# Performance work log

Measured on AMD Instinct MI355X. Metric: run time of the kernel, lower is better.

The kernel has to match this reference:

```python
import jax, jax.numpy as jnp
import numpy as np

DROPOUT_P = 0.0  # undefined global `dropout_p` in source; pinned to 0 (identity) for determinism


def setup_inputs() -> dict:
    key = jax.random.key(0)
    k1, k2, k3 = jax.random.split(key, 3)
    B, Lq, Lk, D = 16, 4096, 4096, 64
    return {
        "query": jax.random.normal(k1, (B, Lq, D), dtype=jnp.float32),
        "key": jax.random.normal(k2, (B, Lk, D), dtype=jnp.float32),
        "value": jax.random.normal(k3, (B, Lk, D), dtype=jnp.float32),
        "scale_factor": jnp.ones((1,), dtype=jnp.float32),
    }


def reference(query, key, value, scale_factor):
    # scores: [B, Lq, Lk] -- the large HBM-materialized intermediate
    scores = jnp.einsum("bqd,bkd->bqk", query, key) / scale_factor
    probs = jax.nn.softmax(scores, axis=-1)
    # dropout with p = DROPOUT_P = 0.0 is the identity
    out = jnp.einsum("bqk,bkd->bqd", probs, value)
    return out
```

## Files before the change

kernel.cpp:

```cpp
#include <hip/hip_runtime.h>
#include <hip/hip_fp16.h>

typedef _Float16 half4_t __attribute__((ext_vector_type(4)));
typedef _Float16 half8_t __attribute__((ext_vector_type(8)));
typedef float   float4_t __attribute__((ext_vector_type(4)));

namespace {
constexpr int kB      = 16;
constexpr int kL      = 4096;
constexpr int kD      = 64;
constexpr int kQTile  = 128;
constexpr int kWQ     = 32;
constexpr int kBK     = 64;
constexpr int kStride = 72;
}

__global__ __launch_bounds__(256, 3)
void fa_fwd(const float* __restrict__ Q, const float* __restrict__ K,
            const float* __restrict__ V, const float* __restrict__ scale_ptr,
            float* __restrict__ Out)
{
    __shared__ __align__(16) _Float16 Ksh[kBK * kStride];
    __shared__ __align__(16) _Float16 Vsh[kD * kStride];

    const int tid  = threadIdx.x;
    const int wave = tid >> 6;
    const int lane = tid & 63;
    const int c    = lane & 15;
    const int qd   = lane >> 4;

    const int b  = blockIdx.y;
    const int q0 = blockIdx.x * kQTile + wave * kWQ;

    const float qscale = 1.4426950408889634f / scale_ptr[0];

    const float* Qb = Q + (size_t)b * kL * kD;
    const float* Kb = K + (size_t)b * kL * kD;
    const float* Vb = V + (size_t)b * kL * kD;

    half8_t qfrag[2][2];
#pragma unroll
    for (int qt = 0; qt < 2; ++qt) {
        const float* qrow = Qb + (size_t)(q0 + qt * 16 + c) * kD;
#pragma unroll
        for (int dk = 0; dk < 2; ++dk) {
            const float* p = qrow + dk * 32 + qd * 8;
            half8_t h;
#pragma unroll
            for (int j = 0; j < 8; ++j) h[j] = (_Float16)(p[j] * qscale);
            qfrag[qt][dk] = h;
        }
    }

    float4_t O[2][4];
#pragma unroll
    for (int qt = 0; qt < 2; ++qt)
#pragma unroll
        for (int dt = 0; dt < 4; ++dt) O[qt][dt] = (float4_t)0.0f;

    float m_run[2] = {-__builtin_inff(), -__builtin_inff()};
    float l_run[2] = {0.0f, 0.0f};

    for (int kb = 0; kb < kL; kb += kBK) {
        __syncthreads();

#pragma unroll
        for (int i = 0; i < 4; ++i) {
            const int task = tid + 256 * i;
            const int c4   = task & 15;
            const int row  = task >> 4;
            const float4 f = *(const float4*)(Kb + (size_t)(kb + row) * kD + c4 * 4);
            half4_t h;
            h[0] = (_Float16)f.x; h[1] = (_Float16)f.y;
            h[2] = (_Float16)f.z; h[3] = (_Float16)f.w;
            *(half4_t*)(&Ksh[row * kStride + c4 * 4]) = h;
        }
#pragma unroll
        for (int i = 0; i < 4; ++i) {
            const int task = tid + 256 * i;
            const int row  = task & 63;
            const int c4   = task >> 6;
            const float4 f = *(const float4*)(Vb + (size_t)(kb + row) * kD + c4 * 4);
            Vsh[(c4 * 4 + 0) * kStride + row] = (_Float16)f.x;
            Vsh[(c4 * 4 + 1) * kStride + row] = (_Float16)f.y;
            Vsh[(c4 * 4 + 2) * kStride + row] = (_Float16)f.z;
            Vsh[(c4 * 4 + 3) * kStride + row] = (_Float16)f.w;
        }
        __syncthreads();

        half8_t kf[4][2];
#pragma unroll
        for (int kt = 0; kt < 4; ++kt)
#pragma unroll
            for (int dk = 0; dk < 2; ++dk)
                kf[kt][dk] = *(const half8_t*)(&Ksh[(kt * 16 + c) * kStride + dk * 32 + qd * 8]);

        float4_t S[4][2];
#pragma unroll
        for (int kt = 0; kt < 4; ++kt)
#pragma unroll
            for (int qt = 0; qt < 2; ++qt) {
                float4_t acc = (float4_t)0.0f;
                acc = __builtin_amdgcn_mfma_f32_16x16x32_f16(kf[kt][0], qfrag[qt][0], acc, 0, 0, 0);
                acc = __builtin_amdgcn_mfma_f32_16x16x32_f16(kf[kt][1], qfrag[qt][1], acc, 0, 0, 0);
                S[kt][qt] = acc;
            }

        float alpha[2];
#pragma unroll
        for (int qt = 0; qt < 2; ++qt) {
            float tm = S[0][qt][0];
#pragma unroll
            for (int kt = 0; kt < 4; ++kt)
#pragma unroll
                for (int r = 0; r < 4; ++r) tm = fmaxf(tm, S[kt][qt][r]);
            tm = fmaxf(tm, __shfl_xor(tm, 16));
            tm = fmaxf(tm, __shfl_xor(tm, 32));
            const float mn = fmaxf(m_run[qt], tm);
            alpha[qt] = __builtin_amdgcn_exp2f(m_run[qt] - mn);
            m_run[qt] = mn;
            float rs = 0.0f;
#pragma unroll
            for (int kt = 0; kt < 4; ++kt)
#pragma unroll
                for (int r = 0; r < 4; ++r) {
                    const float pv = __builtin_amdgcn_exp2f(S[kt][qt][r] - mn);
                    S[kt][qt][r] = pv;
                    rs += pv;
                }
            rs += __shfl_xor(rs, 16);
            rs += __shfl_xor(rs, 32);
            l_run[qt] = l_run[qt] * alpha[qt] + rs;
        }

#pragma unroll
        for (int qt = 0; qt < 2; ++qt)
#pragma unroll
            for (int r = 0; r < 4; ++r) {
                const float a = __shfl(alpha[qt], qd * 4 + r);
#pragma unroll
                for (int dt = 0; dt < 4; ++dt) O[qt][dt][r] *= a;
            }

        half4_t pf[4][2];
#pragma unroll
        for (int kt = 0; kt < 4; ++kt)
#pragma unroll
            for (int qt = 0; qt < 2; ++qt) {
                half4_t h;
                h[0] = (_Float16)S[kt][qt][0]; h[1] = (_Float16)S[kt][qt][1];
                h[2] = (_Float16)S[kt][qt][2]; h[3] = (_Float16)S[kt][qt][3];
                pf[kt][qt] = h;
            }

#pragma unroll
        for (int kt = 0; kt < 4; ++kt)
#pragma unroll
            for (int dt = 0; dt < 4; ++dt) {
                const half4_t vf = *(const half4_t*)(&Vsh[(dt * 16 + c) * kStride + kt * 16 + qd * 4]);
#pragma unroll
                for (int qt = 0; qt < 2; ++qt)
                    O[qt][dt] = __builtin_amdgcn_mfma_f32_16x16x16f16(pf[kt][qt], vf, O[qt][dt], 0, 0, 0);
            }
    }

#pragma unroll
    for (int qt = 0; qt < 2; ++qt)
#pragma unroll
        for (int r = 0; r < 4; ++r) {
            const float lr  = __shfl(l_run[qt], qd * 4 + r);
            const float inv = 1.0f / lr;
            const int qrow  = q0 + qt * 16 + qd * 4 + r;
            float* op = Out + ((size_t)b * kL + qrow) * kD;
#pragma unroll
            for (int dt = 0; dt < 4; ++dt)
                op[dt * 16 + c] = O[qt][dt][r] * inv;
        }
}

extern "C" void kernel_launch(void* const* d_in, const int* in_sizes, int n_in,
                              void* d_out, int out_size, void* d_ws, size_t ws_size,
                              hipStream_t stream) {
    const float* Q = (const float*)d_in[0];
    const float* K = (const float*)d_in[1];
    const float* V = (const float*)d_in[2];
    const float* s = (const float*)d_in[3];
    float* out = (float*)d_out;
    dim3 grid(kL / kQTile, kB, 1);
    dim3 block(256, 1, 1);
    fa_fwd<<<grid, block, 0, stream>>>(Q, K, V, s, out);
}
```

Baseline: 228.8 us.

## Split query tile across eight waves and skip rescale when row max unchanged

Doubles the block to 512 threads so each wave owns 16 query rows instead of 32, halving per-wave registers and raising the launch-bounds occupancy target. The O rescale is skipped via a wave ballot when no row max increased. The row-sum cross-lane reduction is deferred to the end, and fp16 conversions use packed cvt_pkrtz. Scores start from a -32 bias that cancels in softmax. The trade-off is that each wave now reads the K/V fragments from LDS for only half as many rows, so LDS traffic per MFMA doubles.

```diff
diff --git a/kernel.cpp b/kernel.cpp
--- a/kernel.cpp
+++ b/kernel.cpp
@@ -1,21 +1,31 @@
 #include <hip/hip_runtime.h>
 #include <hip/hip_fp16.h>
 
+typedef _Float16 half2_t __attribute__((ext_vector_type(2)));
 typedef _Float16 half4_t __attribute__((ext_vector_type(4)));
 typedef _Float16 half8_t __attribute__((ext_vector_type(8)));
 typedef float   float4_t __attribute__((ext_vector_type(4)));
+
+static __device__ __forceinline__ half2_t cvt_pk(float a, float b) {
+    return __builtin_bit_cast(half2_t, __builtin_amdgcn_cvt_pkrtz(a, b));
+}
+static __device__ __forceinline__ half4_t cvt_pk4(float a, float b, float c, float d) {
+    half2_t lo = cvt_pk(a, b), hi = cvt_pk(c, d);
+    half4_t r;
+    r[0] = lo[0]; r[1] = lo[1]; r[2] = hi[0]; r[3] = hi[1];
+    return r;
+}
 
 namespace {
 constexpr int kB      = 16;
 constexpr int kL      = 4096;
 constexpr int kD      = 64;
 constexpr int kQTile  = 128;
-constexpr int kWQ     = 32;
 constexpr int kBK     = 64;
 constexpr int kStride = 72;
 }
 
-__global__ __launch_bounds__(256, 3)
+__global__ __launch_bounds__(512, 4)
 void fa_fwd(const float* __restrict__ Q, const float* __restrict__ K,
             const float* __restrict__ V, const float* __restrict__ scale_ptr,
             float* __restrict__ Out)
@@ -30,7 +40,7 @@
     const int qd   = lane >> 4;
 
     const int b  = blockIdx.y;
-    const int q0 = blockIdx.x * kQTile + wave * kWQ;
+    const int q0 = blockIdx.x * kQTile + wave * 16;
 
     const float qscale = 1.4426950408889634f / scale_ptr[0];
 
@@ -38,46 +48,40 @@
     const float* Kb = K + (size_t)b * kL * kD;
     const float* Vb = V + (size_t)b * kL * kD;
 
-    half8_t qfrag[2][2];
-#pragma unroll
-    for (int qt = 0; qt < 2; ++qt) {
-        const float* qrow = Qb + (size_t)(q0 + qt * 16 + c) * kD;
+    half8_t qfrag[2];
+    {
+        const float* qrow = Qb + (size_t)(q0 + c) * kD;
 #pragma unroll
         for (int dk = 0; dk < 2; ++dk) {
             const float* p = qrow + dk * 32 + qd * 8;
             half8_t h;
 #pragma unroll
             for (int j = 0; j < 8; ++j) h[j] = (_Float16)(p[j] * qscale);
-            qfrag[qt][dk] = h;
+            qfrag[dk] = h;
         }
     }
 
-    float4_t O[2][4];
+    float4_t O[4];
 #pragma unroll
-    for (int qt = 0; qt < 2; ++qt)
-#pragma unroll
-        for (int dt = 0; dt < 4; ++dt) O[qt][dt] = (float4_t)0.0f;
+    for (int dt = 0; dt < 4; ++dt) O[dt] = (float4_t)0.0f;
 
-    float m_run[2] = {-__builtin_inff(), -__builtin_inff()};
-    float l_run[2] = {0.0f, 0.0f};
+    float m_run = -__builtin_inff();
+    float lpart = 0.0f;
 
     for (int kb = 0; kb < kL; kb += kBK) {
         __syncthreads();
 
 #pragma unroll
-        for (int i = 0; i < 4; ++i) {
-            const int task = tid + 256 * i;
+        for (int i = 0; i < 2; ++i) {
+            const int task = tid + 512 * i;
             const int c4   = task & 15;
             const int row  = task >> 4;
             const float4 f = *(const float4*)(Kb + (size_t)(kb + row) * kD + c4 * 4);
-            half4_t h;
-            h[0] = (_Float16)f.x; h[1] = (_Float16)f.y;
-            h[2] = (_Float16)f.z; h[3] = (_Float16)f.w;
-            *(half4_t*)(&Ksh[row * kStride + c4 * 4]) = h;
+            *(half4_t*)(&Ksh[row * kStride + c4 * 4]) = cvt_pk4(f.x, f.y, f.z, f.w);
         }
 #pragma unroll
-        for (int i = 0; i < 4; ++i) {
-            const int task = tid + 256 * i;
+        for (int i = 0; i < 2; ++i) {
+            const int task = tid + 512 * i;
             const int row  = task & 63;
             const int c4   = task >> 6;
             const float4 f = *(const float4*)(Vb + (size_t)(kb + row) * kD + c4 * 4);
@@ -95,87 +99,71 @@
             for (int dk = 0; dk < 2; ++dk)
                 kf[kt][dk] = *(const half8_t*)(&Ksh[(kt * 16 + c) * kStride + dk * 32 + qd * 8]);
 
-        float4_t S[4][2];
+        float4_t S[4];
+#pragma unroll
+        for (int kt = 0; kt < 4; ++kt) {
+            float4_t acc = {-32.0f, -32.0f, -32.0f, -32.0f};
+            acc = __builtin_amdgcn_mfma_f32_16x16x32_f16(kf[kt][0], qfrag[0], acc, 0, 0, 0);
+            acc = __builtin_amdgcn_mfma_f32_16x16x32_f16(kf[kt][1], qfrag[1], acc, 0, 0, 0);
+            S[kt] = acc;
+        }
+
+        float tm = S[0][0];
 #pragma unroll
         for (int kt = 0; kt < 4; ++kt)
 #pragma unroll
-            for (int qt = 0; qt < 2; ++qt) {
-                float4_t acc = (float4_t)0.0f;
-                acc = __builtin_amdgcn_mfma_f32_16x16x32_f16(kf[kt][0], qfrag[qt][0], acc, 0, 0, 0);
-                acc = __builtin_amdgcn_mfma_f32_16x16x32_f16(kf[kt][1], qfrag[qt][1], acc, 0, 0, 0);
-                S[kt][qt] = acc;
+            for (int r = 0; r < 4; ++r) tm = fmaxf(tm, S[kt][r]);
+        tm = fmaxf(tm, __shfl_xor(tm, 16));
+        tm = fmaxf(tm, __shfl_xor(tm, 32));
+
+        const bool newmax = tm > m_run;
+        const unsigned long long upd = __ballot(newmax);
+        const float mn = newmax ? tm : m_run;
+        if (upd) {
+            const float alpha = __builtin_amdgcn_exp2f(m_run - mn);
+            m_run = mn;
+            lpart *= alpha;
+#pragma unroll
+            for (int r = 0; r < 4; ++r) {
+                const float a = __shfl(alpha, qd * 4 + r);
+#pragma unroll
+                for (int dt = 0; dt < 4; ++dt) O[dt][r] *= a;
             }
-
-        float alpha[2];
-#pragma unroll
-        for (int qt = 0; qt < 2; ++qt) {
-            float tm = S[0][qt][0];
-#pragma unroll
-            for (int kt = 0; kt < 4; ++kt)
-#pragma unroll
-                for (int r = 0; r < 4; ++r) tm = fmaxf(tm, S[kt][qt][r]);
-            tm = fmaxf(tm, __shfl_xor(tm, 16));
-            tm = fmaxf(tm, __shfl_xor(tm, 32));
-            const float mn = fmaxf(m_run[qt], tm);
-            alpha[qt] = __builtin_amdgcn_exp2f(m_run[qt] - mn);
-            m_run[qt] = mn;
-            float rs = 0.0f;
-#pragma unroll
-            for (int kt = 0; kt < 4; ++kt)
-#pragma unroll
-                for (int r = 0; r < 4; ++r) {
-                    const float pv = __builtin_amdgcn_exp2f(S[kt][qt][r] - mn);
-                    S[kt][qt][r] = pv;
-                    rs += pv;
-                }
-            rs += __shfl_xor(rs, 16);
-            rs += __shfl_xor(rs, 32);
-            l_run[qt] = l_run[qt] * alpha[qt] + rs;
         }
 
+        half4_t pf[4];
 #pragma unroll
-        for (int qt = 0; qt < 2; ++qt)
-#pragma unroll
-            for (int r = 0; r < 4; ++r) {
-                const float a = __shfl(alpha[qt], qd * 4 + r);
-#pragma unroll
-                for (int dt = 0; dt < 4; ++dt) O[qt][dt][r] *= a;
-            }
-
-        half4_t pf[4][2];
-#pragma unroll
-        for (int kt = 0; kt < 4; ++kt)
-#pragma unroll
-            for (int qt = 0; qt < 2; ++qt) {
-                half4_t h;
-                h[0] = (_Float16)S[kt][qt][0]; h[1] = (_Float16)S[kt][qt][1];
-                h[2] = (_Float16)S[kt][qt][2]; h[3] = (_Float16)S[kt][qt][3];
-                pf[kt][qt] = h;
-            }
+        for (int kt = 0; kt < 4; ++kt) {
+            float p0 = __builtin_amdgcn_exp2f(S[kt][0] - mn);
+            float p1 = __builtin_amdgcn_exp2f(S[kt][1] - mn);
+            float p2 = __builtin_amdgcn_exp2f(S[kt][2] - mn);
+            float p3 = __builtin_amdgcn_exp2f(S[kt][3] - mn);
+            lpart += (p0 + p1) + (p2 + p3);
+            pf[kt] = cvt_pk4(p0, p1, p2, p3);
+        }
 
 #pragma unroll
         for (int kt = 0; kt < 4; ++kt)
 #pragma unroll
             for (int dt = 0; dt < 4; ++dt) {
                 const half4_t vf = *(const half4_t*)(&Vsh[(dt * 16 + c) * kStride + kt * 16 + qd * 4]);
-#pragma unroll
-                for (int qt = 0; qt < 2; ++qt)
-                    O[qt][dt] = __builtin_amdgcn_mfma_f32_16x16x16f16(pf[kt][qt], vf, O[qt][dt], 0, 0, 0);
+                O[dt] = __builtin_amdgcn_mfma_f32_16x16x16f16(pf[kt], vf, O[dt], 0, 0, 0);
             }
     }
 
+    lpart += __shfl_xor(lpart, 16);
+    lpart += __shfl_xor(lpart, 32);
+
 #pragma unroll
-    for (int qt = 0; qt < 2; ++qt)
+    for (int r = 0; r < 4; ++r) {
+        const float lr  = __shfl(lpart, qd * 4 + r);
+        const float inv = 1.0f / lr;
+        const int qrow  = q0 + qd * 4 + r;
+        float* op = Out + ((size_t)b * kL + qrow) * kD;
 #pragma unroll
-        for (int r = 0; r < 4; ++r) {
-            const float lr  = __shfl(l_run[qt], qd * 4 + r);
-            const float inv = 1.0f / lr;
-            const int qrow  = q0 + qt * 16 + qd * 4 + r;
-            float* op = Out + ((size_t)b * kL + qrow) * kD;
-#pragma unroll
-            for (int dt = 0; dt < 4; ++dt)
-                op[dt * 16 + c] = O[qt][dt][r] * inv;
-        }
+        for (int dt = 0; dt < 4; ++dt)
+            op[dt * 16 + c] = O[dt][r] * inv;
+    }
 }
 
 extern "C" void kernel_launch(void* const* d_in, const int* in_sizes, int n_in,
@@ -187,6 +175,6 @@
     const float* s = (const float*)d_in[3];
     float* out = (float*)d_out;
     dim3 grid(kL / kQTile, kB, 1);
-    dim3 block(256, 1, 1);
+    dim3 block(512, 1, 1);
     fa_fwd<<<grid, block, 0, stream>>>(Q, K, V, s, out);
 }
```

Result: no change. 229.4 us (+0.2%).

## Prefetch next K/V tile into registers and skip O rescale when max unchanged

Applied to the files above, without the earlier changes.

Loads the next K/V tile into registers while computing on the current shared-memory tile, hiding global load latency. The output accumulator is rescaled only when some lane's running max increases, and the row-sum cross-lane reduction is deferred to the epilogue. Conversions use packed cvt_pkrtz, and launch bounds drop to 2 waves per SIMD to fit the extra prefetch registers, at the cost of lower occupancy.

```diff
diff --git a/kernel.cpp b/kernel.cpp
--- a/kernel.cpp
+++ b/kernel.cpp
@@ -1,21 +1,31 @@
 #include <hip/hip_runtime.h>
 #include <hip/hip_fp16.h>
 
+typedef _Float16 half2_t __attribute__((ext_vector_type(2)));
 typedef _Float16 half4_t __attribute__((ext_vector_type(4)));
 typedef _Float16 half8_t __attribute__((ext_vector_type(8)));
 typedef float   float4_t __attribute__((ext_vector_type(4)));
+
+static __device__ __forceinline__ half2_t cvt_pk(float a, float b) {
+    return __builtin_bit_cast(half2_t, __builtin_amdgcn_cvt_pkrtz(a, b));
+}
+static __device__ __forceinline__ half4_t cvt_pk4(float a, float b, float c, float d) {
+    half2_t lo = cvt_pk(a, b), hi = cvt_pk(c, d);
+    half4_t r;
+    r[0] = lo[0]; r[1] = lo[1]; r[2] = hi[0]; r[3] = hi[1];
+    return r;
+}
 
 namespace {
 constexpr int kB      = 16;
 constexpr int kL      = 4096;
 constexpr int kD      = 64;
 constexpr int kQTile  = 128;
-constexpr int kWQ     = 32;
 constexpr int kBK     = 64;
 constexpr int kStride = 72;
 }
 
-__global__ __launch_bounds__(256, 3)
+__global__ __launch_bounds__(256, 2)
 void fa_fwd(const float* __restrict__ Q, const float* __restrict__ K,
             const float* __restrict__ V, const float* __restrict__ scale_ptr,
             float* __restrict__ Out)
@@ -30,7 +40,7 @@
     const int qd   = lane >> 4;
 
     const int b  = blockIdx.y;
-    const int q0 = blockIdx.x * kQTile + wave * kWQ;
+    const int q0 = blockIdx.x * kQTile + wave * 32;
 
     const float qscale = 1.4426950408889634f / scale_ptr[0];
 
@@ -59,34 +69,48 @@
         for (int dt = 0; dt < 4; ++dt) O[qt][dt] = (float4_t)0.0f;
 
     float m_run[2] = {-__builtin_inff(), -__builtin_inff()};
-    float l_run[2] = {0.0f, 0.0f};
+    float lpart[2] = {0.0f, 0.0f};
+
+    float4 pk[4], pv[4];
+#pragma unroll
+    for (int i = 0; i < 4; ++i) {
+        const int tk = tid + 256 * i;
+        pk[i] = *(const float4*)(Kb + (size_t)(tk >> 4) * kD + (tk & 15) * 4);
+        pv[i] = *(const float4*)(Vb + (size_t)(tk & 63) * kD + (tk >> 6) * 4);
+    }
 
     for (int kb = 0; kb < kL; kb += kBK) {
         __syncthreads();
 
 #pragma unroll
         for (int i = 0; i < 4; ++i) {
-            const int task = tid + 256 * i;
-            const int c4   = task & 15;
-            const int row  = task >> 4;
-            const float4 f = *(const float4*)(Kb + (size_t)(kb + row) * kD + c4 * 4);
-            half4_t h;
-            h[0] = (_Float16)f.x; h[1] = (_Float16)f.y;
-            h[2] = (_Float16)f.z; h[3] = (_Float16)f.w;
-            *(half4_t*)(&Ksh[row * kStride + c4 * 4]) = h;
+            const int tk = tid + 256 * i;
+            *(half4_t*)(&Ksh[(tk >> 4) * kStride + (tk & 15) * 4]) =
+                cvt_pk4(pk[i].x, pk[i].y, pk[i].z, pk[i].w);
         }
 #pragma unroll
         for (int i = 0; i < 4; ++i) {
-            const int task = tid + 256 * i;
-            const int row  = task & 63;
-            const int c4   = task >> 6;
-            const float4 f = *(const float4*)(Vb + (size_t)(kb + row) * kD + c4 * 4);
-            Vsh[(c4 * 4 + 0) * kStride + row] = (_Float16)f.x;
-            Vsh[(c4 * 4 + 1) * kStride + row] = (_Float16)f.y;
-            Vsh[(c4 * 4 + 2) * kStride + row] = (_Float16)f.z;
-            Vsh[(c4 * 4 + 3) * kStride + row] = (_Float16)f.w;
+            const int tk  = tid + 256 * i;
+            const int row = tk & 63;
+            const int c4  = tk >> 6;
+            Vsh[(c4 * 4 + 0) * kStride + row] = (_Float16)pv[i].x;
+            Vsh[(c4 * 4 + 1) * kStride + row] = (_Float16)pv[i].y;
+            Vsh[(c4 * 4 + 2) * kStride + row] = (_Float16)pv[i].z;
+            Vsh[(c4 * 4 + 3) * kStride + row] = (_Float16)pv[i].w;
         }
         __syncthreads();
+
+        {
+            const int nb = (kb + kBK) & (kL - 1);
+            const float* Kn = Kb + (size_t)nb * kD;
+            const float* Vn = Vb + (size_t)nb * kD;
+#pragma unroll
+            for (int i = 0; i < 4; ++i) {
+                const int tk = tid + 256 * i;
+                pk[i] = *(const float4*)(Kn + (size_t)(tk >> 4) * kD + (tk & 15) * 4);
+                pv[i] = *(const float4*)(Vn + (size_t)(tk & 63) * kD + (tk >> 6) * 4);
+            }
+        }
 
         half8_t kf[4][2];
 #pragma unroll
@@ -100,13 +124,13 @@
         for (int kt = 0; kt < 4; ++kt)
 #pragma unroll
             for (int qt = 0; qt < 2; ++qt) {
-                float4_t acc = (float4_t)0.0f;
+                float4_t acc = {-32.0f, -32.0f, -32.0f, -32.0f};
                 acc = __builtin_amdgcn_mfma_f32_16x16x32_f16(kf[kt][0], qfrag[qt][0], acc, 0, 0, 0);
                 acc = __builtin_amdgcn_mfma_f32_16x16x32_f16(kf[kt][1], qfrag[qt][1], acc, 0, 0, 0);
                 S[kt][qt] = acc;
             }
 
-        float alpha[2];
+        half4_t pf[4][2];
 #pragma unroll
         for (int qt = 0; qt < 2; ++qt) {
             float tm = S[0][qt][0];
@@ -116,42 +140,31 @@
                 for (int r = 0; r < 4; ++r) tm = fmaxf(tm, S[kt][qt][r]);
             tm = fmaxf(tm, __shfl_xor(tm, 16));
             tm = fmaxf(tm, __shfl_xor(tm, 32));
-            const float mn = fmaxf(m_run[qt], tm);
-            alpha[qt] = __builtin_amdgcn_exp2f(m_run[qt] - mn);
-            m_run[qt] = mn;
-            float rs = 0.0f;
-#pragma unroll
-            for (int kt = 0; kt < 4; ++kt)
+
+            const bool newmax = tm > m_run[qt];
+            const float mn = newmax ? tm : m_run[qt];
+            if (__ballot(newmax)) {
+                const float alpha = __builtin_amdgcn_exp2f(m_run[qt] - mn);
+                m_run[qt] = mn;
+                lpart[qt] *= alpha;
 #pragma unroll
                 for (int r = 0; r < 4; ++r) {
-                    const float pv = __builtin_amdgcn_exp2f(S[kt][qt][r] - mn);
-                    S[kt][qt][r] = pv;
-                    rs += pv;
+                    const float a = __shfl(alpha, qd * 4 + r);
+#pragma unroll
+                    for (int dt = 0; dt < 4; ++dt) O[qt][dt][r] *= a;
                 }
-            rs += __shfl_xor(rs, 16);
-            rs += __shfl_xor(rs, 32);
-            l_run[qt] = l_run[qt] * alpha[qt] + rs;
-        }
-
-#pragma unroll
-        for (int qt = 0; qt < 2; ++qt)
-#pragma unroll
-            for (int r = 0; r < 4; ++r) {
-                const float a = __shfl(alpha[qt], qd * 4 + r);
-#pragma unroll
-                for (int dt = 0; dt < 4; ++dt) O[qt][dt][r] *= a;
-            }
-
-        half4_t pf[4][2];
-#pragma unroll
-        for (int kt = 0; kt < 4; ++kt)
-#pragma unroll
-            for (int qt = 0; qt < 2; ++qt) {
-                half4_t h;
-                h[0] = (_Float16)S[kt][qt][0]; h[1] = (_Float16)S[kt][qt][1];
-                h[2] = (_Float16)S[kt][qt][2]; h[3] = (_Float16)S[kt][qt][3];
-                pf[kt][qt] = h;
-            }
+            }
+
+#pragma unroll
+            for (int kt = 0; kt < 4; ++kt) {
+                const float p0 = __builtin_amdgcn_exp2f(S[kt][qt][0] - mn);
+                const float p1 = __builtin_amdgcn_exp2f(S[kt][qt][1] - mn);
+                const float p2 = __builtin_amdgcn_exp2f(S[kt][qt][2] - mn);
+                const float p3 = __builtin_amdgcn_exp2f(S[kt][qt][3] - mn);
+                lpart[qt] += (p0 + p1) + (p2 + p3);
+                pf[kt][qt] = cvt_pk4(p0, p1, p2, p3);
+            }
+        }
 
 #pragma unroll
         for (int kt = 0; kt < 4; ++kt)
@@ -165,10 +178,16 @@
     }
 
 #pragma unroll
+    for (int qt = 0; qt < 2; ++qt) {
+        lpart[qt] += __shfl_xor(lpart[qt], 16);
+        lpart[qt] += __shfl_xor(lpart[qt], 32);
+    }
+
+#pragma unroll
     for (int qt = 0; qt < 2; ++qt)
 #pragma unroll
         for (int r = 0; r < 4; ++r) {
-            const float lr  = __shfl(l_run[qt], qd * 4 + r);
+            const float lr  = __shfl(lpart[qt], qd * 4 + r);
             const float inv = 1.0f / lr;
             const int qrow  = q0 + qt * 16 + qd * 4 + r;
             float* op = Out + ((size_t)b * kL + qrow) * kD;
```

Measured after the change: 214.3 us. 6.4% less time.
